# Performance work log

Measured on AMD Instinct MI355X. Metric: run time of the kernel, lower is better.

The kernel has to match this reference:

```python
import jax, jax.numpy as jnp
import numpy as np
import math

B, CIN, H, W = 4, 256, 64, 64
COUT = 64
K = 7  # out_kernel


def setup_inputs() -> dict:
    key = jax.random.key(0)
    ks = jax.random.split(key, 9)
    s = 0.05
    x = jax.random.normal(ks[0], (B, CIN, H, W), dtype=jnp.float32)
    Wq = jax.random.normal(ks[1], (COUT, CIN), dtype=jnp.float32) * s
    bq = jax.random.normal(ks[2], (COUT,), dtype=jnp.float32) * s
    Wk = jax.random.normal(ks[3], (COUT, CIN), dtype=jnp.float32) * s
    bk = jax.random.normal(ks[4], (COUT,), dtype=jnp.float32) * s
    Wv = jax.random.normal(ks[5], (COUT, CIN), dtype=jnp.float32) * s
    bv = jax.random.normal(ks[6], (COUT,), dtype=jnp.float32) * s
    Wout = jax.random.normal(ks[7], (COUT, COUT, K, K), dtype=jnp.float32) * s
    bout = jax.random.normal(ks[8], (COUT,), dtype=jnp.float32) * s
    return {"x": x, "Wq": Wq, "bq": bq, "Wk": Wk, "bk": bk,
            "Wv": Wv, "bv": bv, "Wout": Wout, "bout": bout}


def reference(x, Wq, bq, Wk, bk, Wv, bv, Wout, bout):
    b, c, h, w = x.shape
    C = Wq.shape[0]
    hw = h * w
    # 1x1 convs -> (b, h, w, C) channels-last
    qs = jnp.einsum('bchw,oc->bhwo', x, Wq) + bq
    ksp = jnp.einsum('bchw,oc->bhwo', x, Wk) + bk
    vs = jnp.einsum('bchw,oc->bhwo', x, Wv) + bv
    # full QK^T attention over all h*w positions
    qk = jnp.einsum('bic,bjc->bij',
                    qs.reshape(b, hw, C), ksp.reshape(b, hw, C)) / math.sqrt(float(C))
    diag = jnp.arange(hw)
    qk = qk.at[:, diag, diag].set(0.0)  # diagonal zeroed BEFORE softmax
    attn = jax.nn.softmax(qk, axis=-1).reshape(b, h, w, h, w)
    # clamped local-window indices (offsets -K//2 .. K//2)
    off = jnp.arange(K) - K // 2
    idx_h = jnp.clip(jnp.arange(h)[:, None] + off[None, :], 0, h - 1)  # (h,K)
    idx_w = jnp.clip(jnp.arange(w)[:, None] + off[None, :], 0, w - 1)  # (w,K)
    # gather attention weights at local neighborhood: (b,h,w,K,K)
    g = jnp.take_along_axis(attn, idx_h[None, :, None, :, None], axis=3)  # (b,h,w,K,w)
    g = jnp.take_along_axis(g, idx_w[None, None, :, None, :], axis=4)     # (b,h,w,K,K)
    # gather V at local neighborhood: (b,h,w,K,K,C)
    vn = vs[:, idx_h]            # (b,h,K,w,C)
    vn = vn[:, :, :, idx_w]      # (b,h,K,w,K,C)
    vn = jnp.transpose(vn, (0, 1, 3, 2, 4, 5))  # (b,h,w,K,K,C)
    # KxK stride-K conv over the (K,K) window == full contraction per pixel
    out = jnp.einsum('bhwij,bhwijc,ocij->bhwo', g, vn, Wout) + bout
    out = jax.nn.relu(out)
    return jnp.transpose(out, (0, 3, 1, 2))  # (b, C, h, w)
```

## Files before the change

### kernel.cpp

```cpp
#include <hip/hip_runtime.h>
#include <hip/hip_bf16.h>
#include <math.h>

#define BATCH 4
#define CIN   256
#define HH    64
#define WW    64
#define HW    4096
#define COUT  64
#define KK    7
#define NTAP  49
#define NSEG  16

#define QSCALE 0.18033688011112042f

typedef __attribute__((ext_vector_type(8))) short bf16x8;
typedef __attribute__((ext_vector_type(4))) float f32x4;
typedef __attribute__((ext_vector_type(4))) unsigned short u16x4;

__global__ void prep_kernel(
    const float* __restrict__ Wq, const float* __restrict__ bq,
    const float* __restrict__ Wk, const float* __restrict__ bk,
    const float* __restrict__ Wv, const float* __restrict__ bv,
    const float* __restrict__ Wout,
    __hip_bfloat16* __restrict__ Wb192, float* __restrict__ bias192,
    __hip_bfloat16* __restrict__ W2b)
{
    const int idx = blockIdx.x * 256 + threadIdx.x;
    if (idx < 192 * 256) {
        const int row = idx >> 8, c = idx & 255;
        float wsrc;
        if (row < 64)       wsrc = Wq[row * 256 + c];
        else if (row < 128) wsrc = Wk[(row - 64) * 256 + c];
        else                wsrc = Wv[(row - 128) * 256 + c];
        Wb192[idx] = __float2bfloat16(wsrc);
        if (c == 0) {
            float bsrc;
            if (row < 64)       bsrc = bq[row];
            else if (row < 128) bsrc = bk[row - 64];
            else                bsrc = bv[row - 128];
            bias192[row] = bsrc;
        }
    } else if (idx < 192 * 256 + COUT * NTAP * COUT) {
        const int j = idx - 192 * 256;
        const int o = j / (NTAP * COUT);
        const int r = j - o * (NTAP * COUT);
        const int t = r >> 6;
        const int c = r & 63;
        W2b[j] = __float2bfloat16(Wout[((size_t)o * COUT + c) * NTAP + t]);
    }
}

__global__ __launch_bounds__(256) void qkv_mfma(
    const float* __restrict__ x,
    const __hip_bfloat16* __restrict__ Wb192, const float* __restrict__ bias192,
    float* __restrict__ v,
    __hip_bfloat16* __restrict__ qh, __hip_bfloat16* __restrict__ kh)
{
    const int blk = blockIdx.x;
    const int b   = blk >> 8;
    const int p0  = (blk & 255) * 16;
    const int tid = threadIdx.x;
    const int wv  = tid >> 6;
    const int l   = tid & 63;
    const int lg  = l >> 4, lr = l & 15;

    __shared__ __attribute__((aligned(16))) __hip_bfloat16 xsh[16 * 256];

    {
        const int c0 = tid >> 2;
        const int p4 = tid & 3;
        const float4* xb4 = (const float4*)(x + ((size_t)b * CIN) * HW + p0);
#pragma unroll
        for (int it = 0; it < 4; ++it) {
            const int cc = c0 + it * 64;
            const float4 xv = xb4[(size_t)cc * (HW / 4) + p4];
            __hip_bfloat16* dst = &xsh[((cc >> 3) * 16) * 8 + (cc & 7)];
            dst[(p4 * 4 + 0) * 8] = __float2bfloat16(xv.x);
            dst[(p4 * 4 + 1) * 8] = __float2bfloat16(xv.y);
            dst[(p4 * 4 + 2) * 8] = __float2bfloat16(xv.z);
            dst[(p4 * 4 + 3) * 8] = __float2bfloat16(xv.w);
        }
    }
    __syncthreads();

    f32x4 acc0 = {0.f,0.f,0.f,0.f}, acc1 = {0.f,0.f,0.f,0.f}, acc2 = {0.f,0.f,0.f,0.f};
    const short* wb  = (const short*)Wb192;
    const short* xs  = (const short*)xsh;

#pragma unroll
    for (int s = 0; s < 8; ++s) {
        const bf16x8 af = *(const bf16x8*)(xs + (size_t)(((s * 4 + lg) * 16 + lr)) * 8);
        const bf16x8 b0 = *(const bf16x8*)(wb + (size_t)((wv * 3 + 0) * 16 + lr) * 256 + s * 32 + lg * 8);
        const bf16x8 b1 = *(const bf16x8*)(wb + (size_t)((wv * 3 + 1) * 16 + lr) * 256 + s * 32 + lg * 8);
        const bf16x8 b2 = *(const bf16x8*)(wb + (size_t)((wv * 3 + 2) * 16 + lr) * 256 + s * 32 + lg * 8);
        acc0 = __builtin_amdgcn_mfma_f32_16x16x32_bf16(af, b0, acc0, 0, 0, 0);
        acc1 = __builtin_amdgcn_mfma_f32_16x16x32_bf16(af, b1, acc1, 0, 0, 0);
        acc2 = __builtin_amdgcn_mfma_f32_16x16x32_bf16(af, b2, acc2, 0, 0, 0);
    }

    f32x4 accs[3] = {acc0, acc1, acc2};
#pragma unroll
    for (int i = 0; i < 3; ++i) {
        const int otile = wv * 3 + i;
        const int kind  = otile >> 2;
        const int o     = (otile & 3) * 16 + lr;
        const float bias = bias192[otile * 16 + lr];
#pragma unroll
        for (int j = 0; j < 4; ++j) {
            const int p = p0 + lg * 4 + j;
            const size_t addr = ((size_t)b * HW + p) * (size_t)COUT + o;
            const float val = accs[i][j] + bias;
            if (kind == 0)      { qh[addr] = __float2bfloat16(val * QSCALE); }
            else if (kind == 1) { kh[addr] = __float2bfloat16(val); }
            else                { v[addr] = val; }
        }
    }
}

__global__ __launch_bounds__(256) void qk_stats_mfma(
    const __hip_bfloat16* __restrict__ qh, const __hip_bfloat16* __restrict__ kh,
    float* __restrict__ s_part)
{
    const int blk   = blockIdx.x;
    const int b     = blk >> 8;
    const int panel = (blk >> 4) & 15;
    const int jseg  = blk & 15;
    const int tid   = threadIdx.x;
    const int w     = tid >> 6;
    const int l     = tid & 63;
    const int lg    = l >> 4;
    const int lr    = l & 15;
    const int R0    = panel * 256 + w * 64;

    const short* qb = (const short*)(qh + ((size_t)b * HW) * COUT);
    const short* kb = (const short*)(kh + ((size_t)b * HW) * COUT);

    bf16x8 a[4][2];
#pragma unroll
    for (int rt = 0; rt < 4; ++rt) {
        a[rt][0] = *(const bf16x8*)(qb + (size_t)(R0 + rt * 16 + lr) * COUT + lg * 8);
        a[rt][1] = *(const bf16x8*)(qb + (size_t)(R0 + rt * 16 + lr) * COUT + 32 + lg * 8);
    }

    float s[4][4];
#pragma unroll
    for (int rt = 0; rt < 4; ++rt)
#pragma unroll
        for (int i = 0; i < 4; ++i) s[rt][i] = 0.f;

    const int j0 = jseg * 256;
    const short* kptr = kb + (size_t)(j0 + lr) * COUT + lg * 8;

    bf16x8 p0 = *(const bf16x8*)(kptr);
    bf16x8 p1 = *(const bf16x8*)(kptr + 32);
    kptr += 16 * COUT;

    for (int it = 0; it < 16; ++it) {
        bf16x8 n0, n1;
        if (it != 15) {
            n0 = *(const bf16x8*)(kptr);
            n1 = *(const bf16x8*)(kptr + 32);
            kptr += 16 * COUT;
        }
        const int jb = j0 + it * 16;
#pragma unroll
        for (int rt = 0; rt < 4; ++rt) {
            f32x4 d = {0.f, 0.f, 0.f, 0.f};
            d = __builtin_amdgcn_mfma_f32_16x16x32_bf16(a[rt][0], p0, d, 0, 0, 0);
            d = __builtin_amdgcn_mfma_f32_16x16x32_bf16(a[rt][1], p1, d, 0, 0, 0);
            if (jb == R0 + rt * 16) {
                d.x = (lr == lg * 4 + 0) ? 0.f : d.x;
                d.y = (lr == lg * 4 + 1) ? 0.f : d.y;
                d.z = (lr == lg * 4 + 2) ? 0.f : d.z;
                d.w = (lr == lg * 4 + 3) ? 0.f : d.w;
            }
            s[rt][0] += exp2f(d.x);
            s[rt][1] += exp2f(d.y);
            s[rt][2] += exp2f(d.z);
            s[rt][3] += exp2f(d.w);
        }
        p0 = n0; p1 = n1;
    }

#pragma unroll
    for (int rt = 0; rt < 4; ++rt) {
#pragma unroll
        for (int off = 1; off < 16; off <<= 1) {
            s[rt][0] += __shfl_xor(s[rt][0], off, 64);
            s[rt][1] += __shfl_xor(s[rt][1], off, 64);
            s[rt][2] += __shfl_xor(s[rt][2], off, 64);
            s[rt][3] += __shfl_xor(s[rt][3], off, 64);
        }
        if (lr == 0) {
            float4 res = {s[rt][0], s[rt][1], s[rt][2], s[rt][3]};
            *(float4*)(s_part + (size_t)jseg * (BATCH * HW) + (size_t)b * HW +
                       R0 + rt * 16 + lg * 4) = res;
        }
    }
}

__global__ __launch_bounds__(256) void gcalc_mfma(
    const __hip_bfloat16* __restrict__ qh, const __hip_bfloat16* __restrict__ kh,
    const float* __restrict__ s_part, float* __restrict__ g)
{
    const int blk = blockIdx.x;
    const int dh  = blk % 7;
    const int bh  = blk / 7;
    const int h   = bh & 63;
    const int b   = bh >> 6;
    const int tid = threadIdx.x;
    const int wv  = tid >> 6;
    const int l   = tid & 63;
    const int lg  = l >> 4, lr = l & 15;

    const int jh = min(max(h + dh - 3, 0), HH - 1);

    __shared__ float Dsh[64][65];
    __shared__ float rsh[64];

    if (tid < 64) {
        float s = 0.f;
        const size_t base = (size_t)b * HW + h * 64 + tid;
#pragma unroll
        for (int seg = 0; seg < NSEG; ++seg)
            s += s_part[(size_t)seg * (BATCH * HW) + base];
        rsh[tid] = 1.0f / s;
    }

    const short* qb = (const short*)(qh + ((size_t)b * HW + h * 64) * COUT);
    const short* kb = (const short*)(kh + ((size_t)b * HW + jh * 64) * COUT);

    const bf16x8 a0 = *(const bf16x8*)(qb + (size_t)(wv * 16 + lr) * COUT + lg * 8);
    const bf16x8 a1 = *(const bf16x8*)(qb + (size_t)(wv * 16 + lr) * COUT + 32 + lg * 8);

#pragma unroll
    for (int ct = 0; ct < 4; ++ct) {
        const bf16x8 b0 = *(const bf16x8*)(kb + (size_t)(ct * 16 + lr) * COUT + lg * 8);
        const bf16x8 b1 = *(const bf16x8*)(kb + (size_t)(ct * 16 + lr) * COUT + 32 + lg * 8);
        f32x4 d = {0.f, 0.f, 0.f, 0.f};
        d = __builtin_amdgcn_mfma_f32_16x16x32_bf16(a0, b0, d, 0, 0, 0);
        d = __builtin_amdgcn_mfma_f32_16x16x32_bf16(a1, b1, d, 0, 0, 0);
        const int row = wv * 16 + lg * 4;
        const int col = ct * 16 + lr;
        Dsh[row + 0][col] = d.x;
        Dsh[row + 1][col] = d.y;
        Dsh[row + 2][col] = d.z;
        Dsh[row + 3][col] = d.w;
    }
    __syncthreads();

    for (int e = tid; e < 64 * 7; e += 256) {
        const int w  = e / 7;
        const int tj = e - w * 7;
        const int jw = min(max(w + tj - 3, 0), WW - 1);
        const float num = (jh == h && jw == w) ? 1.0f : exp2f(Dsh[w][jw]);
        g[((size_t)b * HW + h * 64 + w) * NTAP + dh * 7 + tj] = num * rsh[w];
    }
}

__global__ __launch_bounds__(256) void out_mfma(
    const float* __restrict__ g, const float* __restrict__ v,
    const __hip_bfloat16* __restrict__ W2b, const float* __restrict__ bout,
    float* __restrict__ out)
{
    const int blk = blockIdx.x;
    const int b   = blk >> 8;
    const int p0  = (blk & 255) * 16;
    const int h   = p0 >> 6;
    const int w0  = p0 & 63;
    const int tid = threadIdx.x;
    const int wv  = tid >> 6;
    const int l   = tid & 63;
    const int lg  = l >> 4, lr = l & 15;

    __shared__ __attribute__((aligned(16))) __hip_bfloat16 gvsh[2][16][72];
    __shared__ float gsh[16][NTAP];

    const int row0 = b * HW + p0;
    for (int i = tid; i < 16 * NTAP; i += 256) {
        const int w = i / NTAP, t = i - w * NTAP;
        gsh[w][t] = g[(size_t)(row0 + w) * NTAP + t];
    }

    const int sw  = tid >> 4;
    const int fc4 = tid & 15;
    const float* vb = v + ((size_t)b * HW) * COUT;

    auto vptr = [&](int t) -> const float4* {
        const int dh = t / 7 - 3, dw = t - (t / 7) * 7 - 3;
        const int jh = min(max(h + dh, 0), HH - 1);
        const int jw = min(max(w0 + sw + dw, 0), WW - 1);
        return (const float4*)(vb + (size_t)((jh << 6) + jw) * COUT) + fc4;
    };

    float4 vv = *vptr(0);
    __syncthreads();

    f32x4 acc = {0.f, 0.f, 0.f, 0.f};
    const short* wrow = (const short*)W2b + (size_t)(wv * 16 + lr) * (NTAP * COUT);

    for (int t = 0; t < NTAP; ++t) {
        const float gg = gsh[sw][t];
        u16x4 pk;
        pk.x = __builtin_bit_cast(unsigned short, __float2bfloat16(vv.x * gg));
        pk.y = __builtin_bit_cast(unsigned short, __float2bfloat16(vv.y * gg));
        pk.z = __builtin_bit_cast(unsigned short, __float2bfloat16(vv.z * gg));
        pk.w = __builtin_bit_cast(unsigned short, __float2bfloat16(vv.w * gg));
        *(u16x4*)(&gvsh[t & 1][sw][fc4 * 4]) = pk;

        float4 vn;
        if (t != NTAP - 1) vn = *vptr(t + 1);

        const bf16x8 B0 = *(const bf16x8*)(wrow + t * 64 + lg * 8);
        const bf16x8 B1 = *(const bf16x8*)(wrow + t * 64 + 32 + lg * 8);

        __syncthreads();
        const short* gsrc = (const short*)&gvsh[t & 1][0][0];
        const bf16x8 A0 = *(const bf16x8*)(gsrc + (size_t)lr * 72 + lg * 8);
        const bf16x8 A1 = *(const bf16x8*)(gsrc + (size_t)lr * 72 + 32 + lg * 8);
        acc = __builtin_amdgcn_mfma_f32_16x16x32_bf16(A0, B0, acc, 0, 0, 0);
        acc = __builtin_amdgcn_mfma_f32_16x16x32_bf16(A1, B1, acc, 0, 0, 0);

        vv = vn;
    }

    const int o  = wv * 16 + lr;
    const float bo = bout[o];
    float4 r;
    r.x = fmaxf(acc.x + bo, 0.f);
    r.y = fmaxf(acc.y + bo, 0.f);
    r.z = fmaxf(acc.z + bo, 0.f);
    r.w = fmaxf(acc.w + bo, 0.f);
    *(float4*)(out + ((size_t)(b * COUT + o) * HW) + p0 + lg * 4) = r;
}

extern "C" void kernel_launch(void* const* d_in, const int* in_sizes, int n_in,
                              void* d_out, int out_size, void* d_ws, size_t ws_size,
                              hipStream_t stream)
{
    const float* x    = (const float*)d_in[0];
    const float* Wq   = (const float*)d_in[1];
    const float* bq   = (const float*)d_in[2];
    const float* Wk   = (const float*)d_in[3];
    const float* bk   = (const float*)d_in[4];
    const float* Wv   = (const float*)d_in[5];
    const float* bv   = (const float*)d_in[6];
    const float* Wout = (const float*)d_in[7];
    const float* bout = (const float*)d_in[8];
    float* out = (float*)d_out;

    float* ws      = (float*)d_ws;
    float* v       = ws;
    float* s_part  = v + (size_t)BATCH * HW * COUT;
    float* g       = s_part + (size_t)NSEG * BATCH * HW;
    float* bias192 = g + (size_t)BATCH * HW * NTAP;
    __hip_bfloat16* qh    = (__hip_bfloat16*)(bias192 + 256);
    __hip_bfloat16* kh    = qh + (size_t)BATCH * HW * COUT;
    __hip_bfloat16* W2b   = kh + (size_t)BATCH * HW * COUT;
    __hip_bfloat16* Wb192 = W2b + (size_t)COUT * NTAP * COUT;

    prep_kernel<<<(192 * 256 + COUT * NTAP * COUT + 255) / 256, 256, 0, stream>>>(
        Wq, bq, Wk, bk, Wv, bv, Wout, Wb192, bias192, W2b);
    qkv_mfma<<<BATCH * (HW / 16), 256, 0, stream>>>(x, Wb192, bias192, v, qh, kh);
    qk_stats_mfma<<<BATCH * 16 * NSEG, 256, 0, stream>>>(qh, kh, s_part);
    gcalc_mfma<<<BATCH * HH * 7, 256, 0, stream>>>(qh, kh, s_part, g);
    out_mfma<<<BATCH * (HW / 16), 256, 0, stream>>>(g, v, W2b, bout, out);
}
```

Measured before the change: 197.7 us.

## Restructure output kernel to stage bf16 V rows in LDS per image row

V is now stored as bf16 instead of fp32. The output kernel is restructured so each block handles a whole image row: it stages 7 neighbouring V rows and the transposed g weights in shared memory once, then runs all 49 taps without per-tap barriers. The g scaling is applied to MFMA partial results (acc += g*d) instead of to the V operand before the bf16 conversion. Each warp computes four output-channel tiles, and results go through LDS for coalesced stores. This removes redundant global V reads and the per-tap syncthreads, at the cost of more MFMAs per tap, high LDS use (about 89 KB), and fewer blocks (256).

```diff
diff --git a/kernel.cpp b/kernel.cpp
--- a/kernel.cpp
+++ b/kernel.cpp
@@ -16,7 +16,6 @@
 
 typedef __attribute__((ext_vector_type(8))) short bf16x8;
 typedef __attribute__((ext_vector_type(4))) float f32x4;
-typedef __attribute__((ext_vector_type(4))) unsigned short u16x4;
 
 __global__ void prep_kernel(
     const float* __restrict__ Wq, const float* __restrict__ bq,
@@ -54,8 +53,8 @@
 __global__ __launch_bounds__(256) void qkv_mfma(
     const float* __restrict__ x,
     const __hip_bfloat16* __restrict__ Wb192, const float* __restrict__ bias192,
-    float* __restrict__ v,
-    __hip_bfloat16* __restrict__ qh, __hip_bfloat16* __restrict__ kh)
+    __hip_bfloat16* __restrict__ qh, __hip_bfloat16* __restrict__ kh,
+    __hip_bfloat16* __restrict__ vh)
 {
     const int blk = blockIdx.x;
     const int b   = blk >> 8;
@@ -113,7 +112,7 @@
             const float val = accs[i][j] + bias;
             if (kind == 0)      { qh[addr] = __float2bfloat16(val * QSCALE); }
             else if (kind == 1) { kh[addr] = __float2bfloat16(val); }
-            else                { v[addr] = val; }
+            else                { vh[addr] = __float2bfloat16(val); }
         }
     }
 }
@@ -260,79 +259,121 @@
 }
 
 __global__ __launch_bounds__(256) void out_mfma(
-    const float* __restrict__ g, const float* __restrict__ v,
+    const float* __restrict__ g, const __hip_bfloat16* __restrict__ vh,
     const __hip_bfloat16* __restrict__ W2b, const float* __restrict__ bout,
     float* __restrict__ out)
 {
     const int blk = blockIdx.x;
-    const int b   = blk >> 8;
-    const int p0  = (blk & 255) * 16;
-    const int h   = p0 >> 6;
-    const int w0  = p0 & 63;
+    const int b   = blk >> 6;
+    const int h   = blk & 63;
     const int tid = threadIdx.x;
-    const int wv  = tid >> 6;
+    const int rt  = tid >> 6;
     const int l   = tid & 63;
     const int lg  = l >> 4, lr = l & 15;
 
-    __shared__ __attribute__((aligned(16))) __hip_bfloat16 gvsh[2][16][72];
-    __shared__ float gsh[16][NTAP];
-
-    const int row0 = b * HW + p0;
-    for (int i = tid; i < 16 * NTAP; i += 256) {
-        const int w = i / NTAP, t = i - w * NTAP;
-        gsh[w][t] = g[(size_t)(row0 + w) * NTAP + t];
-    }
-
-    const int sw  = tid >> 4;
-    const int fc4 = tid & 15;
-    const float* vb = v + ((size_t)b * HW) * COUT;
-
-    auto vptr = [&](int t) -> const float4* {
-        const int dh = t / 7 - 3, dw = t - (t / 7) * 7 - 3;
-        const int jh = min(max(h + dh, 0), HH - 1);
-        const int jw = min(max(w0 + sw + dw, 0), WW - 1);
-        return (const float4*)(vb + (size_t)((jh << 6) + jw) * COUT) + fc4;
-    };
-
-    float4 vv = *vptr(0);
+    __shared__ __attribute__((aligned(16))) __hip_bfloat16 vsh[3640 * 8];
+    __shared__ __attribute__((aligned(16))) float gshT[NTAP * 68];
+    __shared__ __attribute__((aligned(16))) float osh[64 * 68];
+
+    {
+        const short* vhs = (const short*)vh + (size_t)b * HW * COUT;
+#pragma unroll
+        for (int k = 0; k < 14; ++k) {
+            const int idx = k * 256 + tid;
+            const int s  = idx & 7;
+            const int w  = (idx >> 3) & 63;
+            const int dh = idx >> 9;
+            const int jh = min(max(h + dh - 3, 0), HH - 1);
+            const bf16x8 val = *(const bf16x8*)(vhs + ((size_t)(jh * 64 + w)) * COUT + s * 8);
+            *(bf16x8*)((short*)vsh + (size_t)((dh * 8 + s) * 65 + w) * 8) = val;
+        }
+    }
+    {
+        const float* grow = g + (size_t)(b * HW + h * 64) * NTAP;
+#pragma unroll
+        for (int k = 0; k < 13; ++k) {
+            const int idx = k * 256 + tid;
+            if (idx < 64 * NTAP) {
+                const int p = idx / NTAP, t = idx - p * NTAP;
+                gshT[t * 68 + p] = grow[idx];
+            }
+        }
+    }
     __syncthreads();
 
-    f32x4 acc = {0.f, 0.f, 0.f, 0.f};
-    const short* wrow = (const short*)W2b + (size_t)(wv * 16 + lr) * (NTAP * COUT);
+    f32x4 acc[4];
+#pragma unroll
+    for (int ot = 0; ot < 4; ++ot) acc[ot] = (f32x4){0.f, 0.f, 0.f, 0.f};
+
+    const short* vs  = (const short*)vsh;
+    const short* wb2 = (const short*)W2b;
+    const int px = rt * 16 + lr;
+
+    bf16x8 Ac0, Ac1, Bc[4][2];
+    f32x4 gc;
+    {
+        const int wc = min(max(px - 3, 0), 63);
+        Ac0 = *(const bf16x8*)(vs + (size_t)((0 + lg) * 65 + wc) * 8);
+        Ac1 = *(const bf16x8*)(vs + (size_t)((4 + lg) * 65 + wc) * 8);
+#pragma unroll
+        for (int ot = 0; ot < 4; ++ot) {
+            const size_t wr = (size_t)(ot * 16 + lr) * (NTAP * COUT);
+            Bc[ot][0] = *(const bf16x8*)(wb2 + wr + lg * 8);
+            Bc[ot][1] = *(const bf16x8*)(wb2 + wr + 32 + lg * 8);
+        }
+        gc = *(const f32x4*)(gshT + rt * 16 + lg * 4);
+    }
 
     for (int t = 0; t < NTAP; ++t) {
-        const float gg = gsh[sw][t];
-        u16x4 pk;
-        pk.x = __builtin_bit_cast(unsigned short, __float2bfloat16(vv.x * gg));
-        pk.y = __builtin_bit_cast(unsigned short, __float2bfloat16(vv.y * gg));
-        pk.z = __builtin_bit_cast(unsigned short, __float2bfloat16(vv.z * gg));
-        pk.w = __builtin_bit_cast(unsigned short, __float2bfloat16(vv.w * gg));
-        *(u16x4*)(&gvsh[t & 1][sw][fc4 * 4]) = pk;
-
-        float4 vn;
-        if (t != NTAP - 1) vn = *vptr(t + 1);
-
-        const bf16x8 B0 = *(const bf16x8*)(wrow + t * 64 + lg * 8);
-        const bf16x8 B1 = *(const bf16x8*)(wrow + t * 64 + 32 + lg * 8);
-
-        __syncthreads();
-        const short* gsrc = (const short*)&gvsh[t & 1][0][0];
-        const bf16x8 A0 = *(const bf16x8*)(gsrc + (size_t)lr * 72 + lg * 8);
-        const bf16x8 A1 = *(const bf16x8*)(gsrc + (size_t)lr * 72 + 32 + lg * 8);
-        acc = __builtin_amdgcn_mfma_f32_16x16x32_bf16(A0, B0, acc, 0, 0, 0);
-        acc = __builtin_amdgcn_mfma_f32_16x16x32_bf16(A1, B1, acc, 0, 0, 0);
-
-        vv = vn;
-    }
-
-    const int o  = wv * 16 + lr;
+        bf16x8 An0, An1, Bn[4][2];
+        f32x4 gn;
+        if (t + 1 < NTAP) {
+            const int tn = t + 1;
+            const int dh = tn / 7, dw = tn - dh * 7 - 3;
+            const int wc = min(max(px + dw, 0), 63);
+            An0 = *(const bf16x8*)(vs + (size_t)((dh * 8 + lg) * 65 + wc) * 8);
+            An1 = *(const bf16x8*)(vs + (size_t)((dh * 8 + 4 + lg) * 65 + wc) * 8);
+#pragma unroll
+            for (int ot = 0; ot < 4; ++ot) {
+                const size_t wr = (size_t)(ot * 16 + lr) * (NTAP * COUT) + tn * 64;
+                Bn[ot][0] = *(const bf16x8*)(wb2 + wr + lg * 8);
+                Bn[ot][1] = *(const bf16x8*)(wb2 + wr + 32 + lg * 8);
+            }
+            gn = *(const f32x4*)(gshT + tn * 68 + rt * 16 + lg * 4);
+        }
+
+#pragma unroll
+        for (int ot = 0; ot < 4; ++ot) {
+            f32x4 d = {0.f, 0.f, 0.f, 0.f};
+            d = __builtin_amdgcn_mfma_f32_16x16x32_bf16(Ac0, Bc[ot][0], d, 0, 0, 0);
+            d = __builtin_amdgcn_mfma_f32_16x16x32_bf16(Ac1, Bc[ot][1], d, 0, 0, 0);
+            acc[ot] += gc * d;
+        }
+
+        Ac0 = An0; Ac1 = An1; gc = gn;
+#pragma unroll
+        for (int ot = 0; ot < 4; ++ot) { Bc[ot][0] = Bn[ot][0]; Bc[ot][1] = Bn[ot][1]; }
+    }
+
+#pragma unroll
+    for (int ot = 0; ot < 4; ++ot)
+        *(f32x4*)(osh + (size_t)(ot * 16 + lr) * 68 + rt * 16 + lg * 4) = acc[ot];
+    __syncthreads();
+
+    const int o  = tid >> 2;
+    const int c4 = tid & 3;
     const float bo = bout[o];
-    float4 r;
-    r.x = fmaxf(acc.x + bo, 0.f);
-    r.y = fmaxf(acc.y + bo, 0.f);
-    r.z = fmaxf(acc.z + bo, 0.f);
-    r.w = fmaxf(acc.w + bo, 0.f);
-    *(float4*)(out + ((size_t)(b * COUT + o) * HW) + p0 + lg * 4) = r;
+    float* obase = out + ((size_t)(b * COUT + o)) * HW + h * 64;
+#pragma unroll
+    for (int i = 0; i < 4; ++i) {
+        const int p = c4 * 16 + i * 4;
+        float4 vo = *(const float4*)(osh + (size_t)o * 68 + p);
+        vo.x = fmaxf(vo.x + bo, 0.f);
+        vo.y = fmaxf(vo.y + bo, 0.f);
+        vo.z = fmaxf(vo.z + bo, 0.f);
+        vo.w = fmaxf(vo.w + bo, 0.f);
+        *(float4*)(obase + p) = vo;
+    }
 }
 
 extern "C" void kernel_launch(void* const* d_in, const int* in_sizes, int n_in,
@@ -351,19 +392,19 @@
     float* out = (float*)d_out;
 
     float* ws      = (float*)d_ws;
-    float* v       = ws;
-    float* s_part  = v + (size_t)BATCH * HW * COUT;
+    float* s_part  = ws;
     float* g       = s_part + (size_t)NSEG * BATCH * HW;
     float* bias192 = g + (size_t)BATCH * HW * NTAP;
     __hip_bfloat16* qh    = (__hip_bfloat16*)(bias192 + 256);
     __hip_bfloat16* kh    = qh + (size_t)BATCH * HW * COUT;
-    __hip_bfloat16* W2b   = kh + (size_t)BATCH * HW * COUT;
+    __hip_bfloat16* vh    = kh + (size_t)BATCH * HW * COUT;
+    __hip_bfloat16* W2b   = vh + (size_t)BATCH * HW * COUT;
     __hip_bfloat16* Wb192 = W2b + (size_t)COUT * NTAP * COUT;
 
     prep_kernel<<<(192 * 256 + COUT * NTAP * COUT + 255) / 256, 256, 0, stream>>>(
         Wq, bq, Wk, bk, Wv, bv, Wout, Wb192, bias192, W2b);
-    qkv_mfma<<<BATCH * (HW / 16), 256, 0, stream>>>(x, Wb192, bias192, v, qh, kh);
+    qkv_mfma<<<BATCH * (HW / 16), 256, 0, stream>>>(x, Wb192, bias192, qh, kh, vh);
     qk_stats_mfma<<<BATCH * 16 * NSEG, 256, 0, stream>>>(qh, kh, s_part);
     gcalc_mfma<<<BATCH * HH * 7, 256, 0, stream>>>(qh, kh, s_part, g);
-    out_mfma<<<BATCH * (HW / 16), 256, 0, stream>>>(g, v, W2b, bout, out);
-}
+    out_mfma<<<BATCH * HH, 256, 0, stream>>>(g, vh, W2b, bout, out);
+}
```

New measurement: 194.0 us. Within noise of the previous version (-1.8%).
